# Kernel optimization log

Hardware: AMD Instinct MI355X
Metric: run time of the kernel (lower is better)

The kernel has to match this reference:

```python
import jax, jax.numpy as jnp
import numpy as np
from jax import lax

PAD_ID = 50256
POOL = 2  # maxout pool size


def setup_inputs() -> dict:
    key = jax.random.key(0)
    ks = jax.random.split(key, 20)
    B, T, S = 32, 64, 400
    V, DW, DM, DE, DK = 50257, 512, 512, 512, 64
    s = 0.02
    return {
        "tgt_seq": jax.random.randint(ks[0], (B, T), 0, V, dtype=jnp.int32),
        "src_seq": jax.random.randint(ks[1], (B, S), 0, V, dtype=jnp.int32),
        "enc_output": jax.random.normal(ks[2], (B, S, DE), dtype=jnp.float32),
        "hidden": jax.random.normal(ks[3], (B, DE), dtype=jnp.float32),
        "word_emb": jax.random.normal(ks[4], (V, DW), dtype=jnp.float32) * s,
        "W_init": jax.random.normal(ks[5], (DE, DM), dtype=jnp.float32) * s,
        "b_init": jnp.zeros((DM,), jnp.float32),
        "Wx": jax.random.normal(ks[6], (DW + DE, 3 * DM), dtype=jnp.float32) * s,
        "Wh": jax.random.normal(ks[7], (DM, 3 * DM), dtype=jnp.float32) * s,
        "bx": jnp.zeros((3 * DM,), jnp.float32),
        "bh": jnp.zeros((3 * DM,), jnp.float32),
        "Wc": jax.random.normal(ks[8], (DE, DK), dtype=jnp.float32) * s,
        "Wq": jax.random.normal(ks[9], (DM, DK), dtype=jnp.float32) * s,
        "w_cov": jax.random.normal(ks[10], (DK,), dtype=jnp.float32) * s,
        "v_att": jax.random.normal(ks[11], (DK,), dtype=jnp.float32) * s,
        "W_copy": jax.random.normal(ks[12], (DE + DM, 1), dtype=jnp.float32) * s,
        "b_copy": jnp.zeros((1,), jnp.float32),
        "W_read": jax.random.normal(ks[13], (DW + DM + DE, DM), dtype=jnp.float32) * s,
        "b_read": jnp.zeros((DM,), jnp.float32),
    }


def _gru_cell(x, h, Wx, Wh, bx, bh):
    gx = x @ Wx + bx
    gh = h @ Wh + bh
    rx, zx, nx = jnp.split(gx, 3, axis=-1)
    rh, zh, nh = jnp.split(gh, 3, axis=-1)
    r = jax.nn.sigmoid(rx + rh)
    z = jax.nn.sigmoid(zx + zh)
    n = jnp.tanh(nx + r * nh)
    return (1.0 - z) * n + z * h


def reference(tgt_seq, src_seq, enc_output, hidden, word_emb, W_init, b_init,
              Wx, Wh, bx, bh, Wc, Wq, w_cov, v_att, W_copy, b_copy, W_read, b_read):
    B, S, DE = enc_output.shape
    T = tgt_seq.shape[1]
    DM = Wh.shape[0]
    dt = enc_output.dtype

    pad_mask = (src_seq == PAD_ID)                       # [B,S]
    h0 = jnp.tanh(hidden @ W_init + b_init)              # DecInit  [B,DM]
    ctx0 = jnp.zeros((B, DE), dt)                        # attn_init
    cov0 = jnp.zeros((B, S), dt)
    precompute = jnp.einsum('bsd,dk->bsk', enc_output, Wc)  # computed once
    emb = jnp.swapaxes(word_emb[tgt_seq], 0, 1)          # [T,B,DW]

    def step(carry, x):
        h, ctx, cov = carry
        e, t = x
        rnn_in = jnp.concatenate([e, ctx], axis=1)       # input feed
        h = _gru_cell(rnn_in, h, Wx, Wh, bx, bh)
        # concat attention with coverage
        energy = jnp.tanh(precompute + (h @ Wq)[:, None, :]
                          + cov[:, :, None] * w_cov)     # [B,S,DK]
        scores = energy @ v_att                          # [B,S]
        scores = jnp.where(pad_mask, jnp.asarray(-1e9, dt), scores)
        attn = jax.nn.softmax(scores, axis=1)
        new_ctx = jnp.einsum('bs,bsd->bd', attn, enc_output)
        avg_cov = cov / jnp.maximum(t, 1).astype(dt)
        cov_loss = jnp.sum(jnp.minimum(attn, avg_cov), axis=1)
        next_cov = cov + attn
        copy_gate = jax.nn.sigmoid(jnp.concatenate([h, new_ctx], 1) @ W_copy + b_copy)
        readout = jnp.concatenate([e, h, new_ctx], 1) @ W_read + b_read
        maxo = readout.reshape(B, DM // POOL, POOL).max(axis=2)
        return (h, new_ctx, next_cov), (maxo, attn, copy_gate, cov_loss)

    (_, ctx_f, _), (pred, attns, gates, cov_losses) = lax.scan(
        step, (h0, ctx0, cov0), (emb, jnp.arange(T)))
    pred = jnp.swapaxes(pred, 0, 1)              # [B,T,DM//POOL]
    copy_pred = jnp.swapaxes(attns, 0, 1)        # [B,T,S]
    copy_gate = jnp.swapaxes(gates, 0, 1)        # [B,T,1]
    coverage_pred = jnp.swapaxes(cov_losses, 0, 1)  # [B,T]
    return (pred, attns[-1], ctx_f, copy_pred, copy_gate, coverage_pred)
```

## Files before the change

kernel.cpp:

```cpp
#include <hip/hip_runtime.h>
#include <cstdint>
#include <cstddef>


#define PAD_ID_C 50256

typedef float f32x4 __attribute__((ext_vector_type(4)));
typedef short bf16x8 __attribute__((ext_vector_type(8)));

__device__ __forceinline__ unsigned short f2bf(float x){
  union { float f; unsigned u; } v; v.f = x;
  unsigned r = (v.u + 0x7FFFu + ((v.u >> 16) & 1u)) >> 16;
  return (unsigned short)r;
}
__device__ __forceinline__ float bf2f(unsigned short h){
  union { unsigned u; float f; } v; v.u = ((unsigned)h) << 16; return v.f;
}
__device__ __forceinline__ float sigm_(float x){ return 1.f/(1.f+__expf(-x)); }
__device__ __forceinline__ float tanh_(float x){ float e=__expf(2.f*x); return 1.f - 2.f/(e+1.f); }

__device__ __forceinline__ void cstf(float* p, float v){
  __hip_atomic_store(p, v, __ATOMIC_RELAXED, __HIP_MEMORY_SCOPE_AGENT);
}
__device__ __forceinline__ void csts(unsigned short* p, unsigned short v){
  __hip_atomic_store(p, v, __ATOMIC_RELAXED, __HIP_MEMORY_SCOPE_AGENT);
}

__device__ __forceinline__ int pkidx(int b, int d){
  return ((((b>>4)*16) + (d>>5))*64 + (((d>>3)&3)*16) + (b&15))*8 + (d&7);
}


__global__ void k_pack(const float* __restrict__ W, unsigned short* __restrict__ pk, int N, int K){
  int ktc = K >> 5;
  int gid = blockIdx.x*256 + threadIdx.x;
  int total = (N>>4)*ktc*64;
  if (gid >= total) return;
  int lane = gid & 63;
  int rem = gid >> 6;
  int kt = rem % ktc, nt = rem / ktc;
  int k0 = kt*32 + (lane>>4)*8;
  int n  = nt*16 + (lane&15);
  #pragma unroll
  for (int j=0;j<8;j++) pk[gid*8+j] = f2bf(W[(k0+j)*N + n]);
}

__global__ void k_misc(const float* __restrict__ Wq, unsigned short* __restrict__ wq_t,
                       int* __restrict__ barz){
  int idx = blockIdx.x*256 + threadIdx.x;
  if (idx < 32768){ int k = idx >> 9, d = idx & 511; wq_t[idx] = f2bf(Wq[d*64+k]); }
  else if (idx < 32768 + 4112) barz[idx - 32768] = 0;
}

__global__ void k_emb(const int* __restrict__ tgt, const float* __restrict__ word_emb,
                      unsigned short* __restrict__ emb_pk){
  int bid = blockIdx.x;
  int t = bid >> 5, b = bid & 31;
  int token = tgt[b*64 + t];
  const float* src = word_emb + (size_t)token*512;
  for (int d = threadIdx.x; d < 512; d += 256){
    int idx = (((t*2 + (b>>4))*16 + (d>>5))*64 + ((d>>3)&3)*16 + (b&15))*8 + (d&7);
    emb_pk[idx] = f2bf(src[d]);
  }
}

__global__ void k_encbf(const float* __restrict__ enc, unsigned short* __restrict__ enc_bf){
  int idx = blockIdx.x*256 + threadIdx.x;
  if (idx < 32*400*512) enc_bf[idx] = f2bf(enc[idx]);
}

__global__ void k_pre(const float* __restrict__ enc, const float* __restrict__ Wc,
                      unsigned short* __restrict__ pre_t){
  __shared__ float part[4][64];
  int bs = blockIdx.x;
  int k = threadIdx.x & 63, dp = threadIdx.x >> 6;
  const float* e = enc + (size_t)bs*512;
  float acc = 0.f;
  for (int d = dp*128; d < dp*128 + 128; d++) acc += e[d]*Wc[d*64+k];
  part[dp][k] = acc;
  __syncthreads();
  if (threadIdx.x < 64){
    float a = part[0][k] + part[1][k] + part[2][k] + part[3][k];
    pre_t[(size_t)bs*64 + k] = f2bf(a);
  }
}

__global__ void k_h0(const float* __restrict__ hidden, const float* __restrict__ W_init,
                     const float* __restrict__ b_init,
                     float* __restrict__ hf0, unsigned short* __restrict__ hpk0,
                     float* __restrict__ cf0, unsigned short* __restrict__ cpk0){
  int b = blockIdx.x, jj = threadIdx.x;
  const float* hv = hidden + b*512;
  float acc = 0.f;
  for (int d=0; d<512; d++) acc += hv[d]*W_init[d*512+jj];
  float h = tanh_(acc + b_init[jj]);
  hf0[b*512+jj] = h;
  hpk0[pkidx(b,jj)] = f2bf(h);
  cf0[b*512+jj] = 0.f;
  cpk0[b*512+jj] = 0;
}

__global__ void k_gxe(const unsigned short* __restrict__ emb_pk,
                      const unsigned short* __restrict__ wxe,
                      const float* __restrict__ bx, const float* __restrict__ bh,
                      float* __restrict__ gxe){
  int job = blockIdx.x*4 + (threadIdx.x>>6);
  int lane = threadIdx.x & 63;
  int nt = job % 96, mtg = job / 96;
  f32x4 acc = {0.f,0.f,0.f,0.f};
  const bf16x8* ae = (const bf16x8*)emb_pk + (size_t)(mtg*16)*64 + lane;
  const bf16x8* wp = (const bf16x8*)wxe + (size_t)(nt*16)*64 + lane;
  #pragma unroll
  for (int kt=0; kt<16; kt++)
    acc = __builtin_amdgcn_mfma_f32_16x16x32_bf16(ae[kt*64], wp[kt*64], acc, 0,0,0);
  int row = mtg*16 + (lane>>4)*4, col = nt*16 + (lane&15);
  float badd = bx[col] + (col < 1024 ? bh[col] : 0.f);
  #pragma unroll
  for (int i=0;i<4;i++) gxe[(size_t)(row+i)*1536 + col] = acc[i] + badd;
}


struct PP {
  const unsigned short *emb, *wxc, *wh, *wr, *wq, *pre, *enc;
  const float *gxe;
  unsigned short *hpk, *cpk;
  float *gx, *gh;
  float *hf, *cf;
  const float *Wcopy, *bcopy, *bh, *bread, *wcov, *vatt;
  const int* src;
  float *out_pred, *out_attnlast, *out_ctxf, *out_copypred, *out_gate, *out_covloss;
  int *arr;
};

__device__ __forceinline__ void gridbar(int* arr, int idx){
  asm volatile("s_waitcnt vmcnt(0) lgkmcnt(0)" ::: "memory");
  __syncthreads();
  if (threadIdx.x == 0)
    __hip_atomic_store(arr + blockIdx.x*16, idx, __ATOMIC_RELAXED, __HIP_MEMORY_SCOPE_AGENT);
  if (threadIdx.x < 256){
    while (__hip_atomic_load(arr + threadIdx.x*16, __ATOMIC_RELAXED, __HIP_MEMORY_SCOPE_AGENT) < idx)
      __builtin_amdgcn_s_sleep(1);
  }
  __syncthreads();
}

__device__ __forceinline__ float blockReduceSum(float v, float* redw, int tid){
  #pragma unroll
  for (int off=32; off; off>>=1) v += __shfl_down(v, off, 64);
  if ((tid & 63) == 0) redw[tid>>6] = v;
  __syncthreads();
  if (tid == 0){
    float r = 0.f;
    #pragma unroll
    for (int i=0;i<8;i++) r += redw[i];
    redw[8] = r;
  }
  __syncthreads();
  return redw[8];
}

__global__ __launch_bounds__(512,1) void k_steps(PP p){
  __shared__ float h_s[512];
  __shared__ float hq_part[8][64];
  __shared__ float hq_s[64];
  __shared__ float wv_s[128];
  __shared__ float p_s[400];
  __shared__ float redw[16];
  __shared__ float cred[64][65];

  const int tid = threadIdx.x;
  const int b = blockIdx.x & 31, g = blockIdx.x >> 5;
  int idx = 0;
  float c_reg = 0.f;

  if (tid < 128) wv_s[tid] = (tid < 64) ? p.wcov[tid] : p.vatt[tid-64];
  h_s[tid] = p.hf[b*512 + tid];
  const bool padv = (tid < 400) ? (p.src[b*400+tid] == PAD_ID_C) : true;
  const float bh2r = p.bh[1024 + tid];
  const float* gxe_b = p.gxe;
  __syncthreads();

  for (int t = 0; t < 64; ++t){
    const unsigned short* hpk_t = p.hpk + (size_t)t*16384;
    const unsigned short* cpk_t = p.cpk + (size_t)t*16384;
    float* gx_t = p.gx + (size_t)t*49152;
    float* gh_t = p.gh + (size_t)t*49152;

    {
      int wib = tid >> 6, lane = tid & 63;
      if (wib < 2){
        int wv = wib*256 + blockIdx.x;
        if (wv < 192){
          int nt = wv % 96, mt = wv / 96;
          f32x4 acc = {0.f,0.f,0.f,0.f};
          const bf16x8* wp = (const bf16x8*)p.wxc + (size_t)(nt*16)*64 + lane;
          const bf16x8* ac = (const bf16x8*)cpk_t + (size_t)(mt*16)*64 + lane;
          #pragma unroll
          for (int kt=0; kt<16; kt++)
            acc = __builtin_amdgcn_mfma_f32_16x16x32_bf16(ac[kt*64], wp[kt*64], acc, 0,0,0);
          int row = mt*16 + (lane>>4)*4, col = nt*16 + (lane&15);
          #pragma unroll
          for (int i=0;i<4;i++) cstf(&gx_t[(row+i)*1536 + col], acc[i]);
        } else if (wv < 384){
          int ww = wv - 192;
          int nt = ww % 96, mt = ww / 96;
          f32x4 acc = {0.f,0.f,0.f,0.f};
          const bf16x8* wp = (const bf16x8*)p.wh + (size_t)(nt*16)*64 + lane;
          const bf16x8* ah = (const bf16x8*)hpk_t + (size_t)(mt*16)*64 + lane;
          #pragma unroll
          for (int kt=0; kt<16; kt++)
            acc = __builtin_amdgcn_mfma_f32_16x16x32_bf16(ah[kt*64], wp[kt*64], acc, 0,0,0);
          int row = mt*16 + (lane>>4)*4, col = nt*16 + (lane&15);
          #pragma unroll
          for (int i=0;i<4;i++) cstf(&gh_t[(row+i)*1536 + col], acc[i]);
        }
      }
    }
    gridbar(p.arr, ++idx);

    float* hf_w = p.hf + (size_t)(t+1)*16384;
    unsigned short* hpk_w = p.hpk + (size_t)(t+1)*16384;
    float* cf_w = p.cf + (size_t)(t+1)*16384;
    unsigned short* cpk_w = p.cpk + (size_t)(t+1)*16384;

    {
      int jj = tid;
      const float* gxer = p.gxe + (size_t)((t*2 + (b>>4))*16 + (b&15))*1536;
      const float* gxr = gx_t + b*1536;
      const float* ghr = gh_t + b*1536;
      float e0 = gxer[jj], e1 = gxer[512+jj], e2 = gxer[1024+jj];
      float x0 = gxr[jj],  x1 = gxr[512+jj],  x2 = gxr[1024+jj];
      float y0 = ghr[jj],  y1 = ghr[512+jj],  y2 = ghr[1024+jj];
      float r = sigm_(e0 + x0 + y0);
      float z = sigm_(e1 + x1 + y1);
      float n = tanh_(e2 + x2 + r*(y2 + bh2r));
      float hold = h_s[jj];
      float hn = (1.f - z)*n + z*hold;
      __syncthreads();
      h_s[jj] = hn;
      if (g == 0){ cstf(&hf_w[b*512+jj], hn); csts(&hpk_w[pkidx(b,jj)], f2bf(hn)); }
    }
    __syncthreads();

    {
      int k = tid & 63, pr = tid >> 6;
      const unsigned short* wrow = p.wq + k*512 + pr*64;
      float a = 0.f;
      #pragma unroll
      for (int c=0;c<8;c++){
        bf16x8 v = *(const bf16x8*)(wrow + c*8);
        #pragma unroll
        for (int j=0;j<8;j++) a += h_s[pr*64 + c*8 + j]*bf2f((unsigned short)v[j]);
      }
      hq_part[pr][k] = a;
    }
    __syncthreads();
    if (tid < 64){
      float a = 0.f;
      #pragma unroll
      for (int pr=0;pr<8;pr++) a += hq_part[pr][tid];
      hq_s[tid] = a;
    }
    __syncthreads();

    float c_old = c_reg, p_val = 0.f;
    if (tid < 400){
      const unsigned short* prow = p.pre + ((size_t)b*400 + tid)*64;
      float a = 0.f;
      #pragma unroll
      for (int kk=0; kk<8; kk++){
        bf16x8 v = *(const bf16x8*)(prow + kk*8);
        #pragma unroll
        for (int j=0;j<8;j++){
          int k = kk*8 + j;
          float e = bf2f((unsigned short)v[j]) + hq_s[k] + c_old*wv_s[k];
          a += tanh_(e)*wv_s[64+k];
        }
      }
      p_val = padv ? 0.f : __expf(a);
      p_s[tid] = p_val;
    }
    float total = blockReduceSum((tid < 400) ? p_val : 0.f, redw, tid);
    float inv_total = 1.f/total;

    float cl = 0.f;
    float inv_t = 1.f/(float)(t < 1 ? 1 : t);
    if (tid < 400){
      float attnv = p_val*inv_total;
      if (g == 0){
        p.out_copypred[((size_t)b*64 + t)*400 + tid] = attnv;
        if (t == 63) p.out_attnlast[b*400+tid] = attnv;
      }
      cl = fminf(attnv, c_old*inv_t);
      c_reg = c_old + attnv;
    }
    float cls = blockReduceSum(cl, redw, tid);
    if (g == 0 && tid == 0) p.out_covloss[b*64 + t] = cls;

    {
      int dv = tid & 7, sp = tid >> 3;
      int dgb = g*64 + dv*8;
      float acc[8] = {0.f,0.f,0.f,0.f,0.f,0.f,0.f,0.f};
      const unsigned short* ebase = p.enc + (size_t)(b*400)*512 + dgb;
      for (int ss = sp; ss < 400; ss += 64){
        bf16x8 v = *(const bf16x8*)(ebase + (size_t)ss*512);
        float pw = p_s[ss];
        #pragma unroll
        for (int j=0;j<8;j++) acc[j] += pw*bf2f((unsigned short)v[j]);
      }
      #pragma unroll
      for (int j=0;j<8;j++) cred[sp][dv*8+j] = acc[j];
    }
    __syncthreads();
    if (tid < 64){
      float cx = 0.f;
      #pragma unroll
      for (int s2=0;s2<64;s2++) cx += cred[s2][tid];
      cx *= inv_total;
      int dg = g*64 + tid;
      cstf(&cf_w[b*512+dg], cx);
      csts(&cpk_w[pkidx(b,dg)], f2bf(cx));
      if (t == 63) p.out_ctxf[b*512+dg] = cx;
    }
    gridbar(p.arr, ++idx);
  }

  {
    int wslot = blockIdx.x*8 + (tid>>6);
    int lane = tid & 63;

    for (int job = wslot; job < 4096; job += 2048){
      int nt = job & 31, mtg = job >> 5;
      int t = mtg >> 1, half = mtg & 1;
      f32x4 acc = {0.f,0.f,0.f,0.f};
      const bf16x8* wp = (const bf16x8*)p.wr + (size_t)(nt*48)*64 + lane;
      const bf16x8* ae = (const bf16x8*)p.emb + (size_t)(mtg*16)*64 + lane;
      const bf16x8* ah = (const bf16x8*)(p.hpk + (size_t)(t+1)*16384) + (size_t)(half*16)*64 + lane;
      const bf16x8* ac = (const bf16x8*)(p.cpk + (size_t)(t+1)*16384) + (size_t)(half*16)*64 + lane;
      #pragma unroll
      for (int kt=0; kt<16; kt++)
        acc = __builtin_amdgcn_mfma_f32_16x16x32_bf16(ae[kt*64], wp[kt*64], acc, 0,0,0);
      #pragma unroll
      for (int kt=0; kt<16; kt++)
        acc = __builtin_amdgcn_mfma_f32_16x16x32_bf16(ah[kt*64], wp[(16+kt)*64], acc, 0,0,0);
      #pragma unroll
      for (int kt=0; kt<16; kt++)
        acc = __builtin_amdgcn_mfma_f32_16x16x32_bf16(ac[kt*64], wp[(32+kt)*64], acc, 0,0,0);
      int colL = nt*16 + (lane&15);
      int b0 = half*16 + ((lane>>4)&3)*4;
      #pragma unroll
      for (int i=0;i<4;i++){
        float v = acc[i] + p.bread[colL];
        float o = __shfl_xor(v, 1, 64);
        if (!(lane & 1)){
          p.out_pred[((size_t)(b0+i)*64 + t)*256 + nt*8 + ((lane&15)>>1)] = fmaxf(v, o);
        }
      }
    }

    {
      int b2 = wslot >> 6, t = wslot & 63;
      const float* hfr = p.hf + (size_t)(t+1)*16384 + b2*512;
      const float* cfr = p.cf + (size_t)(t+1)*16384 + b2*512;
      float acc = 0.f;
      #pragma unroll
      for (int i=0;i<16;i++){
        int j = i*64 + lane;
        float x = (j < 512) ? hfr[j] : cfr[j-512];
        acc += x * p.Wcopy[j];
      }
      #pragma unroll
      for (int off=32; off>0; off>>=1) acc += __shfl_down(acc, off, 64);
      if (lane == 0) p.out_gate[b2*64 + t] = sigm_(acc + p.bcopy[0]);
    }
  }
}

extern "C" void kernel_launch(void* const* d_in, const int* in_sizes, int n_in,
                              void* d_out, int out_size, void* d_ws, size_t ws_size,
                              hipStream_t stream) {
  const int*   tgt     = (const int*)  d_in[0];
  const int*   src     = (const int*)  d_in[1];
  const float* enc     = (const float*)d_in[2];
  const float* hidden  = (const float*)d_in[3];
  const float* wemb    = (const float*)d_in[4];
  const float* W_init  = (const float*)d_in[5];
  const float* b_init  = (const float*)d_in[6];
  const float* Wx      = (const float*)d_in[7];
  const float* Wh      = (const float*)d_in[8];
  const float* bx      = (const float*)d_in[9];
  const float* bh      = (const float*)d_in[10];
  const float* Wc      = (const float*)d_in[11];
  const float* Wq      = (const float*)d_in[12];
  const float* w_cov   = (const float*)d_in[13];
  const float* v_att   = (const float*)d_in[14];
  const float* W_copy  = (const float*)d_in[15];
  const float* b_copy  = (const float*)d_in[16];
  const float* W_read  = (const float*)d_in[17];
  const float* b_read  = (const float*)d_in[18];

  float* out0 = (float*)d_out;
  float* out1 = out0 + 524288;
  float* out2 = out0 + 537088;
  float* out3 = out0 + 553472;
  float* out4 = out0 + 1372672;
  float* out5 = out0 + 1374720;

  uint8_t* w = (uint8_t*)d_ws;
  unsigned short* emb_pk = (unsigned short*)(w);
  unsigned short* enc_bf = (unsigned short*)(w + 2097152);
  unsigned short* pre_t  = (unsigned short*)(w + 15204352);
  unsigned short* wxe_pk = (unsigned short*)(w + 16842752);
  unsigned short* wxc_pk = (unsigned short*)(w + 18415616);
  unsigned short* wh_pk  = (unsigned short*)(w + 19988480);
  unsigned short* wr_pk  = (unsigned short*)(w + 21561344);
  unsigned short* wq_t   = (unsigned short*)(w + 23134208);
  float* gxe    = (float*)(w + 23199744);
  float* gx_sl  = (float*)(w + 35782656);
  float* gh_sl  = (float*)(w + 48365568);
  unsigned short* hpk_sl = (unsigned short*)(w + 60948480);
  unsigned short* cpk_sl = (unsigned short*)(w + 63078400);
  float* hf_sl  = (float*)(w + 65208320);
  float* cf_sl  = (float*)(w + 69468160);
  int*   arr    = (int*)  (w + 73728000);

  k_pack<<<384, 256, 0, stream>>>(Wx, wxe_pk, 1536, 512);
  k_pack<<<384, 256, 0, stream>>>(Wx + (size_t)512*1536, wxc_pk, 1536, 512);
  k_pack<<<384, 256, 0, stream>>>(Wh, wh_pk, 1536, 512);
  k_pack<<<384, 256, 0, stream>>>(W_read, wr_pk, 512, 1536);
  k_misc<<<145, 256, 0, stream>>>(Wq, wq_t, arr);
  k_emb<<<2048, 256, 0, stream>>>(tgt, wemb, emb_pk);
  k_encbf<<<25600, 256, 0, stream>>>(enc, enc_bf);
  k_pre<<<12800, 256, 0, stream>>>(enc, Wc, pre_t);
  k_h0<<<32, 512, 0, stream>>>(hidden, W_init, b_init, hf_sl, hpk_sl, cf_sl, cpk_sl);
  k_gxe<<<3072, 256, 0, stream>>>(emb_pk, wxe_pk, bx, bh, gxe);

  PP p;
  p.emb = emb_pk; p.wxc = wxc_pk; p.wh = wh_pk; p.wr = wr_pk; p.wq = wq_t;
  p.pre = pre_t; p.enc = enc_bf; p.gxe = gxe;
  p.hpk = hpk_sl; p.cpk = cpk_sl;
  p.gx = gx_sl; p.gh = gh_sl;
  p.hf = hf_sl; p.cf = cf_sl;
  p.Wcopy = W_copy; p.bcopy = b_copy; p.bh = bh; p.bread = b_read;
  p.wcov = w_cov; p.vatt = v_att; p.src = src;
  p.out_pred = out0; p.out_attnlast = out1; p.out_ctxf = out2;
  p.out_copypred = out3; p.out_gate = out4; p.out_covloss = out5;
  p.arr = arr;

  void* kargs[] = { (void*)&p };
  hipLaunchCooperativeKernel((const void*)k_steps, dim3(256), dim3(512), kargs, 0, stream);
}
```

Before: 1.698 ms.

## Fuse x/h gate GEMMs per wave, prefetch gxe to LDS, cache Wq in registers

Each block's single wave now computes both the context-input and hidden gate MFMA tiles together and writes pre-summed r/z gates into one combined buffer, so the GRU update reads fewer global values. Other waves prefetch the block's precomputed embedding gate row into shared memory before the grid barrier, and Wq rows are held in registers across all steps instead of being reloaded every step. The barrier spin drops s_sleep, and output writes are spread across blocks by thread group instead of always coming from group 0. This trades more register pressure and busier barrier polling for less global traffic and latency on the serial step path.

```diff
diff --git a/kernel.cpp b/kernel.cpp
--- a/kernel.cpp
+++ b/kernel.cpp
@@ -124,7 +124,7 @@
   const unsigned short *emb, *wxc, *wh, *wr, *wq, *pre, *enc;
   const float *gxe;
   unsigned short *hpk, *cpk;
-  float *gx, *gh;
+  float *gb;
   float *hf, *cf;
   const float *Wcopy, *bcopy, *bh, *bread, *wcov, *vatt;
   const int* src;
@@ -138,8 +138,7 @@
   if (threadIdx.x == 0)
     __hip_atomic_store(arr + blockIdx.x*16, idx, __ATOMIC_RELAXED, __HIP_MEMORY_SCOPE_AGENT);
   if (threadIdx.x < 256){
-    while (__hip_atomic_load(arr + threadIdx.x*16, __ATOMIC_RELAXED, __HIP_MEMORY_SCOPE_AGENT) < idx)
-      __builtin_amdgcn_s_sleep(1);
+    while (__hip_atomic_load(arr + threadIdx.x*16, __ATOMIC_RELAXED, __HIP_MEMORY_SCOPE_AGENT) < idx){}
   }
   __syncthreads();
 }
@@ -161,6 +160,7 @@
 
 __global__ __launch_bounds__(512,1) void k_steps(PP p){
   __shared__ float h_s[512];
+  __shared__ float gxe_s[1536];
   __shared__ float hq_part[8][64];
   __shared__ float hq_s[64];
   __shared__ float wv_s[128];
@@ -177,43 +177,51 @@
   h_s[tid] = p.hf[b*512 + tid];
   const bool padv = (tid < 400) ? (p.src[b*400+tid] == PAD_ID_C) : true;
   const float bh2r = p.bh[1024 + tid];
-  const float* gxe_b = p.gxe;
+  const int sown = tid/50 == g ? 1 : 0;
+  bf16x8 wqreg[8];
+  {
+    int k = tid & 63, pr = tid >> 6;
+    const bf16x8* wrow = (const bf16x8*)(p.wq + k*512 + pr*64);
+    #pragma unroll
+    for (int c=0;c<8;c++) wqreg[c] = wrow[c];
+  }
   __syncthreads();
 
   for (int t = 0; t < 64; ++t){
     const unsigned short* hpk_t = p.hpk + (size_t)t*16384;
     const unsigned short* cpk_t = p.cpk + (size_t)t*16384;
-    float* gx_t = p.gx + (size_t)t*49152;
-    float* gh_t = p.gh + (size_t)t*49152;
+    float* gb_t = p.gb + (size_t)t*65536;
 
     {
       int wib = tid >> 6, lane = tid & 63;
-      if (wib < 2){
-        int wv = wib*256 + blockIdx.x;
-        if (wv < 192){
-          int nt = wv % 96, mt = wv / 96;
-          f32x4 acc = {0.f,0.f,0.f,0.f};
-          const bf16x8* wp = (const bf16x8*)p.wxc + (size_t)(nt*16)*64 + lane;
+      if (wib == 0){
+        if (blockIdx.x < 192){
+          int nt = blockIdx.x % 96, mt = blockIdx.x / 96;
+          f32x4 aX = {0.f,0.f,0.f,0.f}, aH = {0.f,0.f,0.f,0.f};
+          const bf16x8* wpX = (const bf16x8*)p.wxc + (size_t)(nt*16)*64 + lane;
+          const bf16x8* wpH = (const bf16x8*)p.wh  + (size_t)(nt*16)*64 + lane;
           const bf16x8* ac = (const bf16x8*)cpk_t + (size_t)(mt*16)*64 + lane;
-          #pragma unroll
-          for (int kt=0; kt<16; kt++)
-            acc = __builtin_amdgcn_mfma_f32_16x16x32_bf16(ac[kt*64], wp[kt*64], acc, 0,0,0);
-          int row = mt*16 + (lane>>4)*4, col = nt*16 + (lane&15);
-          #pragma unroll
-          for (int i=0;i<4;i++) cstf(&gx_t[(row+i)*1536 + col], acc[i]);
-        } else if (wv < 384){
-          int ww = wv - 192;
-          int nt = ww % 96, mt = ww / 96;
-          f32x4 acc = {0.f,0.f,0.f,0.f};
-          const bf16x8* wp = (const bf16x8*)p.wh + (size_t)(nt*16)*64 + lane;
           const bf16x8* ah = (const bf16x8*)hpk_t + (size_t)(mt*16)*64 + lane;
           #pragma unroll
-          for (int kt=0; kt<16; kt++)
-            acc = __builtin_amdgcn_mfma_f32_16x16x32_bf16(ah[kt*64], wp[kt*64], acc, 0,0,0);
+          for (int kt=0; kt<16; kt++){
+            aX = __builtin_amdgcn_mfma_f32_16x16x32_bf16(ac[kt*64], wpX[kt*64], aX, 0,0,0);
+            aH = __builtin_amdgcn_mfma_f32_16x16x32_bf16(ah[kt*64], wpH[kt*64], aH, 0,0,0);
+          }
           int row = mt*16 + (lane>>4)*4, col = nt*16 + (lane&15);
-          #pragma unroll
-          for (int i=0;i<4;i++) cstf(&gh_t[(row+i)*1536 + col], acc[i]);
+          if (col < 1024){
+            #pragma unroll
+            for (int i=0;i<4;i++) cstf(&gb_t[(row+i)*2048 + col], aX[i]+aH[i]);
+          } else {
+            #pragma unroll
+            for (int i=0;i<4;i++){
+              cstf(&gb_t[(row+i)*2048 + col], aX[i]);
+              cstf(&gb_t[(row+i)*2048 + col + 512], aH[i]);
+            }
+          }
         }
+      } else {
+        const float* gxer = p.gxe + (size_t)((t*2 + (b>>4))*16 + (b&15))*1536;
+        for (int i = tid - 64; i < 1536; i += 448) gxe_s[i] = gxer[i];
       }
     }
     gridbar(p.arr, ++idx);
@@ -225,32 +233,27 @@
 
     {
       int jj = tid;
-      const float* gxer = p.gxe + (size_t)((t*2 + (b>>4))*16 + (b&15))*1536;
-      const float* gxr = gx_t + b*1536;
-      const float* ghr = gh_t + b*1536;
-      float e0 = gxer[jj], e1 = gxer[512+jj], e2 = gxer[1024+jj];
-      float x0 = gxr[jj],  x1 = gxr[512+jj],  x2 = gxr[1024+jj];
-      float y0 = ghr[jj],  y1 = ghr[512+jj],  y2 = ghr[1024+jj];
-      float r = sigm_(e0 + x0 + y0);
-      float z = sigm_(e1 + x1 + y1);
+      const float* gbr = gb_t + b*2048;
+      float s0 = gbr[jj], s1 = gbr[512+jj], x2 = gbr[1024+jj], y2 = gbr[1536+jj];
+      float e0 = gxe_s[jj], e1 = gxe_s[512+jj], e2 = gxe_s[1024+jj];
+      float r = sigm_(e0 + s0);
+      float z = sigm_(e1 + s1);
       float n = tanh_(e2 + x2 + r*(y2 + bh2r));
       float hold = h_s[jj];
       float hn = (1.f - z)*n + z*hold;
       __syncthreads();
       h_s[jj] = hn;
-      if (g == 0){ cstf(&hf_w[b*512+jj], hn); csts(&hpk_w[pkidx(b,jj)], f2bf(hn)); }
+      if ((tid>>6) == g){ cstf(&hf_w[b*512+jj], hn); csts(&hpk_w[pkidx(b,jj)], f2bf(hn)); }
     }
     __syncthreads();
 
     {
       int k = tid & 63, pr = tid >> 6;
-      const unsigned short* wrow = p.wq + k*512 + pr*64;
       float a = 0.f;
       #pragma unroll
       for (int c=0;c<8;c++){
-        bf16x8 v = *(const bf16x8*)(wrow + c*8);
         #pragma unroll
-        for (int j=0;j<8;j++) a += h_s[pr*64 + c*8 + j]*bf2f((unsigned short)v[j]);
+        for (int j=0;j<8;j++) a += h_s[pr*64 + c*8 + j]*bf2f((unsigned short)wqreg[c][j]);
       }
       hq_part[pr][k] = a;
     }
@@ -287,7 +290,7 @@
     float inv_t = 1.f/(float)(t < 1 ? 1 : t);
     if (tid < 400){
       float attnv = p_val*inv_total;
-      if (g == 0){
+      if (sown){
         p.out_copypred[((size_t)b*64 + t)*400 + tid] = attnv;
         if (t == 63) p.out_attnlast[b*400+tid] = attnv;
       }
@@ -347,7 +350,7 @@
       for (int kt=0; kt<16; kt++)
         acc = __builtin_amdgcn_mfma_f32_16x16x32_bf16(ac[kt*64], wp[(32+kt)*64], acc, 0,0,0);
       int colL = nt*16 + (lane&15);
-      int b0 = half*16 + ((lane>>4)&3)*4;
+      int b0 = half*16 + (lane>>4)*4;
       #pragma unroll
       for (int i=0;i<4;i++){
         float v = acc[i] + p.bread[colL];
@@ -416,13 +419,12 @@
   unsigned short* wr_pk  = (unsigned short*)(w + 21561344);
   unsigned short* wq_t   = (unsigned short*)(w + 23134208);
   float* gxe    = (float*)(w + 23199744);
-  float* gx_sl  = (float*)(w + 35782656);
-  float* gh_sl  = (float*)(w + 48365568);
-  unsigned short* hpk_sl = (unsigned short*)(w + 60948480);
-  unsigned short* cpk_sl = (unsigned short*)(w + 63078400);
-  float* hf_sl  = (float*)(w + 65208320);
-  float* cf_sl  = (float*)(w + 69468160);
-  int*   arr    = (int*)  (w + 73728000);
+  float* gb_sl  = (float*)(w + 35782656);
+  unsigned short* hpk_sl = (unsigned short*)(w + 52559872);
+  unsigned short* cpk_sl = (unsigned short*)(w + 54689792);
+  float* hf_sl  = (float*)(w + 56819712);
+  float* cf_sl  = (float*)(w + 61079552);
+  int*   arr    = (int*)  (w + 65339392);
 
   k_pack<<<384, 256, 0, stream>>>(Wx, wxe_pk, 1536, 512);
   k_pack<<<384, 256, 0, stream>>>(Wx + (size_t)512*1536, wxc_pk, 1536, 512);
@@ -439,7 +441,7 @@
   p.emb = emb_pk; p.wxc = wxc_pk; p.wh = wh_pk; p.wr = wr_pk; p.wq = wq_t;
   p.pre = pre_t; p.enc = enc_bf; p.gxe = gxe;
   p.hpk = hpk_sl; p.cpk = cpk_sl;
-  p.gx = gx_sl; p.gh = gh_sl;
+  p.gb = gb_sl;
   p.hf = hf_sl; p.cf = cf_sl;
   p.Wcopy = W_copy; p.bcopy = b_copy; p.bh = bh; p.bread = b_read;
   p.wcov = w_cov; p.vatt = v_att; p.src = src;
```

Result: no change. 1.689 ms (-0.5%).
